# Kernel tuning notes

Measured on AMD Instinct MI355X. Metric: run time of the kernel, lower is better.

Reference implementation:

```python
import jax, jax.numpy as jnp
import numpy as np

F_REP = 256
F_BET = 512
N_PER = 6
MAGNITUDE = 0.001


def _glorot(key, shape):
    fan_in = shape[0]
    return jax.random.normal(key, shape, dtype=jnp.float32) / np.sqrt(fan_in)


def setup_inputs() -> dict:
    key = jax.random.key(0)
    ks = jax.random.split(key, 24)
    n_atoms, n_tors = 50000, 300000
    inp = {
        'h': jax.random.normal(ks[0], (n_atoms, F_REP), dtype=jnp.float32),
        'idxs': jax.random.randint(ks[1], (n_tors, 4), 0, n_atoms, dtype=jnp.int64),
        # symmetrizer: skippedLinear(4*rep, bet) + DenseBlock(bet, depth=3)
        'Ws0': _glorot(ks[2], (4 * F_REP, F_BET)), 'bs0': jnp.zeros((F_BET,), jnp.float32),
        'Ws1': _glorot(ks[3], (F_BET, F_BET)), 'bs1': jnp.zeros((F_BET,), jnp.float32),
        'Ws2': _glorot(ks[4], (F_BET, F_BET)), 'bs2': jnp.zeros((F_BET,), jnp.float32),
        'Ws3': _glorot(ks[5], (F_BET, F_BET)), 'bs3': jnp.zeros((F_BET,), jnp.float32),
        # torsion_nn: DenseBlock(bet, depth=2) + Linear(bet, n_periodicity)
        'Wt0': _glorot(ks[6], (F_BET, F_BET)), 'bt0': jnp.zeros((F_BET,), jnp.float32),
        'Wt1': _glorot(ks[7], (F_BET, F_BET)), 'bt1': jnp.zeros((F_BET,), jnp.float32),
        'Wt2': _glorot(ks[8], (F_BET, N_PER)), 'bt2': jnp.zeros((N_PER,), jnp.float32),
        # classification_nn: skippedLinear(bet, bet) + Linear(bet, n_periodicity)
        'Wc0': _glorot(ks[9], (F_BET, F_BET)), 'bc0': jnp.zeros((F_BET,), jnp.float32),
        'Wc1': _glorot(ks[10], (F_BET, N_PER)), 'bc1': jnp.zeros((N_PER,), jnp.float32),
    }
    return inp


def _symmetrizer(x, Ws0, bs0, Ws1, bs1, Ws2, bs2, Ws3, bs3):
    # skippedLinear(4*rep, bet): dims differ -> plain Linear + ELU
    h = jax.nn.elu(x @ Ws0 + bs0)
    # DenseBlock: residual Linear+ELU layers (in==out)
    for W, b in ((Ws1, bs1), (Ws2, bs2), (Ws3, bs3)):
        h = h + jax.nn.elu(h @ W + b)
    return h


def reference(h, idxs, Ws0, bs0, Ws1, bs1, Ws2, bs2, Ws3, bs3,
              Wt0, bt0, Wt1, bt1, Wt2, bt2, Wc0, bc0, Wc1, bc1):
    feats = h[idxs]  # [N, 4, F_REP] gather
    f1, f2, f3, f4 = feats[:, 0], feats[:, 1], feats[:, 2], feats[:, 3]
    x_fwd = jnp.concatenate([f1, f2, f3, f4], axis=-1)  # [N, 4F]
    x_rev = jnp.concatenate([f4, f3, f2, f1], axis=-1)
    sym = (_symmetrizer(x_fwd, Ws0, bs0, Ws1, bs1, Ws2, bs2, Ws3, bs3)
           + _symmetrizer(x_rev, Ws0, bs0, Ws1, bs1, Ws2, bs2, Ws3, bs3))
    # torsion_nn
    t = sym + jax.nn.elu(sym @ Wt0 + bt0)
    t = t + jax.nn.elu(t @ Wt1 + bt1)
    coeffs = t @ Wt2 + bt2  # [N, n_periodicity]
    # classification_nn (skippedLinear with in==out -> residual)
    c = sym + jax.nn.elu(sym @ Wc0 + bc0)
    score = c @ Wc1 + bc1  # [N, n_periodicity]
    gate = jax.nn.sigmoid(score)  # hardness == 1
    k = coeffs * MAGNITUDE * gate
    return jnp.stack([score, k])  # [2, N, n_periodicity]
```

## Files before the change

kernel.cpp:

```cpp
#include <hip/hip_runtime.h>

#define BM 64
#define NTHREADS 512
#define BM4 32
#define NT4 1024

typedef __attribute__((ext_vector_type(8))) short short8;
typedef __attribute__((ext_vector_type(4))) float f32x4;

__device__ __forceinline__ short f2bf(float f) {
  unsigned u = __builtin_bit_cast(unsigned, f);
  u += 0x7FFFu + ((u >> 16) & 1u);
  return (short)(u >> 16);
}
__device__ __forceinline__ float bf2f(short s) {
  unsigned u = ((unsigned)(unsigned short)s) << 16;
  return __builtin_bit_cast(float, u);
}
__device__ __forceinline__ float elu_f(float v) {
  return v > 0.f ? v : (__expf(v) - 1.f);
}

__global__ __launch_bounds__(256) void pack_w(const float* __restrict__ src,
                                              short* __restrict__ dst,
                                              int K, int N, int rev) {
  int tile = blockIdx.x * 4 + (threadIdx.x >> 6);
  int lane = threadIdx.x & 63;
  int ktiles = K >> 5;
  int tot = (N >> 4) * ktiles;
  if (tile >= tot) return;
  int nt = tile / ktiles, kt = tile - nt * ktiles;
  int col = (nt << 4) + (lane & 15);
  int k0 = (kt << 5) + ((lane >> 4) << 3);
  short8 o;
#pragma unroll
  for (int j = 0; j < 8; ++j) {
    int kr = k0 + j;
    if (rev) kr = ((3 - (kr >> 8)) << 8) | (kr & 255);
    o[j] = f2bf(src[(size_t)kr * N + col]);
  }
  *(short8*)(dst + (size_t)tile * 512 + lane * 8) = o;
}

__device__ __forceinline__ short8 ldg_bfrag(const short* W, int ktiles, int ct,
                                            int kt, int lane) {
  return *(const short8*)(W + ((size_t)(ct * ktiles + kt) << 9) + (lane << 3));
}

__device__ __forceinline__ int swz(int row, int boff) {
  return row * 1024 + (boff ^ ((row & 7) << 4) ^ (((row >> 3) & 1) << 7));
}
__device__ __forceinline__ short8 lds_a32(const char* base, int rt, int kt, int lane) {
  int row = rt * 16 + (lane & 15);
  int boff = (kt << 6) + ((lane >> 4) << 4);
  return *(const short8*)(base + swz(row, boff));
}

__device__ __forceinline__ short8 lds_afrag64(const char* base, int stride, int rt,
                                              int kt, int lane) {
  int row = rt * 16 + (lane & 15);
  int boff = (kt << 6) + ((lane >> 4) << 4);
  return *(const short8*)(base + row * stride + (boff ^ ((row & 7) << 4)));
}

__global__ __launch_bounds__(NTHREADS) void atom_pre(const float* __restrict__ h,
                                                     const short* __restrict__ W0f,
                                                     short* __restrict__ p,
                                                     int n_atoms) {
  __shared__ char sh[BM * 512];
  const int tid = threadIdx.x, lane = tid & 63, wv = tid >> 6;
  const int r0 = blockIdx.x * BM;
  for (int i = tid; i < BM * 32; i += NTHREADS) {
    int row = i >> 5, c0 = (i & 31) << 3;
    int ga = r0 + row;
    short8 o;
    if (ga < n_atoms) {
      const float4* s4 = (const float4*)(h + (size_t)ga * 256 + c0);
      float4 v0 = s4[0], v1 = s4[1];
      o[0] = f2bf(v0.x); o[1] = f2bf(v0.y); o[2] = f2bf(v0.z); o[3] = f2bf(v0.w);
      o[4] = f2bf(v1.x); o[5] = f2bf(v1.y); o[6] = f2bf(v1.z); o[7] = f2bf(v1.w);
    } else {
#pragma unroll
      for (int e = 0; e < 8; ++e) o[e] = 0;
    }
    *(short8*)(sh + row * 512 + ((c0 * 2) ^ ((row & 7) << 4))) = o;
  }
  __syncthreads();
#pragma unroll 1
  for (int s = 0; s < 4; ++s) {
    f32x4 acc[4][4];
    const f32x4 z = {0.f, 0.f, 0.f, 0.f};
#pragma unroll
    for (int rt = 0; rt < 4; ++rt)
#pragma unroll
      for (int cf = 0; cf < 4; ++cf) acc[rt][cf] = z;
    for (int kt = 0; kt < 8; ++kt) {
      short8 a[4], b[4];
#pragma unroll
      for (int rt = 0; rt < 4; ++rt) a[rt] = lds_afrag64(sh, 512, rt, kt, lane);
#pragma unroll
      for (int cf = 0; cf < 4; ++cf)
        b[cf] = ldg_bfrag(W0f, 32, (wv << 2) + cf, (s << 3) + kt, lane);
#pragma unroll
      for (int rt = 0; rt < 4; ++rt)
#pragma unroll
        for (int cf = 0; cf < 4; ++cf)
          acc[rt][cf] = __builtin_amdgcn_mfma_f32_16x16x32_bf16(a[rt], b[cf], acc[rt][cf], 0, 0, 0);
    }
#pragma unroll
    for (int rt = 0; rt < 4; ++rt)
#pragma unroll
      for (int cf = 0; cf < 4; ++cf) {
        int col = (wv << 6) + (cf << 4) + (lane & 15);
#pragma unroll
        for (int i = 0; i < 4; ++i) {
          int row = rt * 16 + ((lane >> 4) << 2) + i;
          int ga = r0 + row;
          if (ga < n_atoms) p[((size_t)ga * 4 + s) * 512 + col] = f2bf(acc[rt][cf][i]);
        }
      }
  }
}

struct P2 {
  const int* idxs;
  const short* p;
  const short *W1, *W2, *W3, *Wt0, *Wt1, *Wc0;
  const float *bs0, *bs1, *bs2, *bs3, *bt0, *bt1, *bt2, *bc0, *bc1;
  const float *Wt2, *Wc1;
  float* out;
  int n_tors;
};


__device__ __forceinline__ void mfma_dual(const char* sA, const char* sB,
                                          const short* __restrict__ W,
                                          const float* __restrict__ bias,
                                          f32x4 (&accf)[2][2], f32x4 (&accr)[2][2],
                                          int wv, int lane) {
  float b0 = bias[(wv << 5) + (lane & 15)];
  float b1 = bias[(wv << 5) + 16 + (lane & 15)];
#pragma unroll
  for (int rt = 0; rt < 2; ++rt) {
    accf[rt][0] = (f32x4){b0, b0, b0, b0};
    accf[rt][1] = (f32x4){b1, b1, b1, b1};
    accr[rt][0] = (f32x4){b0, b0, b0, b0};
    accr[rt][1] = (f32x4){b1, b1, b1, b1};
  }
  short8 bC[2], bN[2];
#pragma unroll
  for (int cf = 0; cf < 2; ++cf) bC[cf] = ldg_bfrag(W, 16, (wv << 1) + cf, 0, lane);
#pragma unroll 1
  for (int kt = 0; kt < 16; ++kt) {
#pragma unroll
    for (int cf = 0; cf < 2; ++cf)
      bN[cf] = ldg_bfrag(W, 16, (wv << 1) + cf, (kt + 1) & 15, lane);
#pragma unroll
    for (int rt = 0; rt < 2; ++rt) {
      short8 af = lds_a32(sA, rt, kt, lane);
      short8 ar = lds_a32(sB, rt, kt, lane);
#pragma unroll
      for (int cf = 0; cf < 2; ++cf) {
        accf[rt][cf] = __builtin_amdgcn_mfma_f32_16x16x32_bf16(af, bC[cf], accf[rt][cf], 0, 0, 0);
        accr[rt][cf] = __builtin_amdgcn_mfma_f32_16x16x32_bf16(ar, bC[cf], accr[rt][cf], 0, 0, 0);
      }
    }
#pragma unroll
    for (int cf = 0; cf < 2; ++cf) bC[cf] = bN[cf];
  }
}

__device__ __forceinline__ void mfma_dualB(const char* sA,
                                           const short* __restrict__ Wa,
                                           const short* __restrict__ Wb,
                                           const float* __restrict__ ba,
                                           const float* __restrict__ bb,
                                           f32x4 (&accA)[2][2], f32x4 (&accB)[2][2],
                                           int wv, int lane) {
  float a0 = ba[(wv << 5) + (lane & 15)];
  float a1 = ba[(wv << 5) + 16 + (lane & 15)];
  float c0 = bb[(wv << 5) + (lane & 15)];
  float c1 = bb[(wv << 5) + 16 + (lane & 15)];
#pragma unroll
  for (int rt = 0; rt < 2; ++rt) {
    accA[rt][0] = (f32x4){a0, a0, a0, a0};
    accA[rt][1] = (f32x4){a1, a1, a1, a1};
    accB[rt][0] = (f32x4){c0, c0, c0, c0};
    accB[rt][1] = (f32x4){c1, c1, c1, c1};
  }
#pragma unroll 1
  for (int kt = 0; kt < 16; ++kt) {
    short8 bA[2], bB[2];
#pragma unroll
    for (int cf = 0; cf < 2; ++cf) {
      bA[cf] = ldg_bfrag(Wa, 16, (wv << 1) + cf, kt, lane);
      bB[cf] = ldg_bfrag(Wb, 16, (wv << 1) + cf, kt, lane);
    }
#pragma unroll
    for (int rt = 0; rt < 2; ++rt) {
      short8 a = lds_a32(sA, rt, kt, lane);
#pragma unroll
      for (int cf = 0; cf < 2; ++cf) {
        accA[rt][cf] = __builtin_amdgcn_mfma_f32_16x16x32_bf16(a, bA[cf], accA[rt][cf], 0, 0, 0);
        accB[rt][cf] = __builtin_amdgcn_mfma_f32_16x16x32_bf16(a, bB[cf], accB[rt][cf], 0, 0, 0);
      }
    }
  }
}

__device__ __forceinline__ void mfma_single(const char* src,
                                            const short* __restrict__ W,
                                            const float* __restrict__ bias,
                                            f32x4 (&acc)[2][2], int wv, int lane) {
  float b0 = bias[(wv << 5) + (lane & 15)];
  float b1 = bias[(wv << 5) + 16 + (lane & 15)];
#pragma unroll
  for (int rt = 0; rt < 2; ++rt) {
    acc[rt][0] = (f32x4){b0, b0, b0, b0};
    acc[rt][1] = (f32x4){b1, b1, b1, b1};
  }
  short8 bC[2], bN[2];
#pragma unroll
  for (int cf = 0; cf < 2; ++cf) bC[cf] = ldg_bfrag(W, 16, (wv << 1) + cf, 0, lane);
#pragma unroll 1
  for (int kt = 0; kt < 16; ++kt) {
#pragma unroll
    for (int cf = 0; cf < 2; ++cf)
      bN[cf] = ldg_bfrag(W, 16, (wv << 1) + cf, (kt + 1) & 15, lane);
#pragma unroll
    for (int rt = 0; rt < 2; ++rt) {
      short8 a = lds_a32(src, rt, kt, lane);
#pragma unroll
      for (int cf = 0; cf < 2; ++cf)
        acc[rt][cf] = __builtin_amdgcn_mfma_f32_16x16x32_bf16(a, bC[cf], acc[rt][cf], 0, 0, 0);
    }
#pragma unroll
    for (int cf = 0; cf < 2; ++cf) bC[cf] = bN[cf];
  }
}

__global__ __launch_bounds__(NT4, 8) void fused4(P2 p) {
  __shared__ char sA[BM4 * 1024];
  __shared__ char sB[BM4 * 1024];
  __shared__ int sIdx[BM4 * 4];
  __shared__ float sSmall[BM4 * 12];
  const int tid = threadIdx.x;
  const int lane = tid & 63;
  const int wv = tid >> 6;
  const int r0 = blockIdx.x * BM4;

  if (tid < BM4 * 4) {
    int grow = r0 + (tid >> 2);
    sIdx[tid] = (grow < p.n_tors) ? p.idxs[(size_t)grow * 4 + (tid & 3)] : 0;
  }
  __syncthreads();

#pragma unroll 1
  for (int i = tid; i < BM4 * 64; i += NT4) {
    int row = i >> 6, c0 = (i & 63) << 3;
    float sf[8], sr[8];
#pragma unroll
    for (int e = 0; e < 8; ++e) { sf[e] = p.bs0[c0 + e]; sr[e] = sf[e]; }
#pragma unroll
    for (int j = 0; j < 4; ++j) {
      int a = sIdx[row * 4 + j];
      short8 vf = *(const short8*)(p.p + ((size_t)a * 4 + j) * 512 + c0);
      short8 vr = *(const short8*)(p.p + ((size_t)a * 4 + (3 - j)) * 512 + c0);
#pragma unroll
      for (int e = 0; e < 8; ++e) { sf[e] += bf2f(vf[e]); sr[e] += bf2f(vr[e]); }
    }
    short8 of, orv;
#pragma unroll
    for (int e = 0; e < 8; ++e) { of[e] = f2bf(elu_f(sf[e])); orv[e] = f2bf(elu_f(sr[e])); }
    int off = swz(row, c0 * 2);
    *(short8*)(sA + off) = of;
    *(short8*)(sB + off) = orv;
  }
  __syncthreads();

  f32x4 accA[2][2], accB[2][2];

  const short* Ws[3] = {p.W1, p.W2, p.W3};
  const float* bs[3] = {p.bs1, p.bs2, p.bs3};
#pragma unroll 1
  for (int L = 0; L < 3; ++L) {
    mfma_dual(sA, sB, Ws[L], bs[L], accA, accB, wv, lane);
    __syncthreads();
#pragma unroll
    for (int rt = 0; rt < 2; ++rt)
#pragma unroll
      for (int cf = 0; cf < 2; ++cf) {
        int col = (wv << 5) + (cf << 4) + (lane & 15);
#pragma unroll
        for (int i = 0; i < 4; ++i) {
          int row = rt * 16 + ((lane >> 4) << 2) + i;
          int off = swz(row, col * 2);
          short* pf = (short*)(sA + off);
          short* pr = (short*)(sB + off);
          float nf = bf2f(*pf) + elu_f(accA[rt][cf][i]);
          float nr = bf2f(*pr) + elu_f(accB[rt][cf][i]);
          if (L == 2) {
            *pf = f2bf(nf + nr);
          } else {
            *pf = f2bf(nf);
            *pr = f2bf(nr);
          }
        }
      }
    __syncthreads();
  }

  mfma_dualB(sA, p.Wt0, p.Wc0, p.bt0, p.bc0, accA, accB, wv, lane);
  __syncthreads();
#pragma unroll
  for (int rt = 0; rt < 2; ++rt)
#pragma unroll
    for (int cf = 0; cf < 2; ++cf) {
      int col = (wv << 5) + (cf << 4) + (lane & 15);
#pragma unroll
      for (int i = 0; i < 4; ++i) {
        int row = rt * 16 + ((lane >> 4) << 2) + i;
        int off = swz(row, col * 2);
        float s = bf2f(*(short*)(sA + off));
        *(short*)(sB + off) = f2bf(s + elu_f(accA[rt][cf][i]));
        *(short*)(sA + off) = f2bf(s + elu_f(accB[rt][cf][i]));
      }
    }
  __syncthreads();

  mfma_single(sB, p.Wt1, p.bt1, accA, wv, lane);
  __syncthreads();
#pragma unroll
  for (int rt = 0; rt < 2; ++rt)
#pragma unroll
    for (int cf = 0; cf < 2; ++cf) {
      int col = (wv << 5) + (cf << 4) + (lane & 15);
#pragma unroll
      for (int i = 0; i < 4; ++i) {
        int row = rt * 16 + ((lane >> 4) << 2) + i;
        int off = swz(row, col * 2);
        short* pt = (short*)(sB + off);
        *pt = f2bf(bf2f(*pt) + elu_f(accA[rt][cf][i]));
      }
    }
  __syncthreads();

  if (tid < BM4 * 12) {
    int row = tid / 12, jj = tid - row * 12;
    int j = (jj < 6) ? jj : jj - 6;
    const char* src = (jj < 6) ? sB : sA;
    const float* W = (jj < 6) ? p.Wt2 : p.Wc1;
    float acc = (jj < 6) ? p.bt2[j] : p.bc1[j];
#pragma unroll 1
    for (int c0 = 0; c0 < 512; c0 += 8) {
      short8 v = *(const short8*)(src + swz(row, c0 * 2));
#pragma unroll
      for (int e = 0; e < 8; ++e) acc += bf2f(v[e]) * W[(c0 + e) * 6 + j];
    }
    sSmall[row * 12 + jj] = acc;
  }
  __syncthreads();
  if (tid < BM4 * 6) {
    int row = tid / 6, j = tid - row * 6;
    int grow = r0 + row;
    if (grow < p.n_tors) {
      float score = sSmall[row * 12 + 6 + j];
      float coeff = sSmall[row * 12 + j];
      p.out[(size_t)grow * 6 + j] = score;
      p.out[(size_t)p.n_tors * 6 + (size_t)grow * 6 + j] =
          coeff * 0.001f * (1.0f / (1.0f + __expf(-score)));
    }
  }
}


struct Params {
  const float* h;
  const int* idxs;
  const short *W0f, *W0r, *W1, *W2, *W3, *Wt0, *Wt1, *Wc0;
  const float *bs0, *bs1, *bs2, *bs3, *bt0, *bt1, *bt2, *bc0, *bc1;
  const float *Wt2, *Wc1;
  float* out;
  int n_tors;
};

__device__ __forceinline__ void layer_dual(char* hf, char* hr,
                                           const short* __restrict__ W,
                                           const float* __restrict__ bias,
                                           int wv, int lane) {
  f32x4 accf[4][4], accr[4][4];
  const f32x4 z = {0.f, 0.f, 0.f, 0.f};
#pragma unroll
  for (int rt = 0; rt < 4; ++rt)
#pragma unroll
    for (int cf = 0; cf < 4; ++cf) { accf[rt][cf] = z; accr[rt][cf] = z; }
  for (int kt = 0; kt < 16; ++kt) {
    short8 af[4], ar[4], b[4];
#pragma unroll
    for (int rt = 0; rt < 4; ++rt) {
      af[rt] = lds_afrag64(hf, 1024, rt, kt, lane);
      ar[rt] = lds_afrag64(hr, 1024, rt, kt, lane);
    }
#pragma unroll
    for (int cf = 0; cf < 4; ++cf) b[cf] = ldg_bfrag(W, 16, (wv << 2) + cf, kt, lane);
#pragma unroll
    for (int rt = 0; rt < 4; ++rt)
#pragma unroll
      for (int cf = 0; cf < 4; ++cf) {
        accf[rt][cf] = __builtin_amdgcn_mfma_f32_16x16x32_bf16(af[rt], b[cf], accf[rt][cf], 0, 0, 0);
        accr[rt][cf] = __builtin_amdgcn_mfma_f32_16x16x32_bf16(ar[rt], b[cf], accr[rt][cf], 0, 0, 0);
      }
  }
  float bcol[4];
#pragma unroll
  for (int cf = 0; cf < 4; ++cf) bcol[cf] = bias[(wv << 6) + (cf << 4) + (lane & 15)];
  __syncthreads();
#pragma unroll
  for (int rt = 0; rt < 4; ++rt)
#pragma unroll
    for (int cf = 0; cf < 4; ++cf) {
      int col = (wv << 6) + (cf << 4) + (lane & 15);
#pragma unroll
      for (int i = 0; i < 4; ++i) {
        int row = rt * 16 + ((lane >> 4) << 2) + i;
        size_t off = (size_t)row * 1024 + ((col * 2) ^ ((row & 7) << 4));
        short* pf = (short*)(hf + off);
        short* pr = (short*)(hr + off);
        *pf = f2bf(bf2f(*pf) + elu_f(accf[rt][cf][i] + bcol[cf]));
        *pr = f2bf(bf2f(*pr) + elu_f(accr[rt][cf][i] + bcol[cf]));
      }
    }
  __syncthreads();
}

__device__ __forceinline__ void layer_single(const char* in,
                                             const short* __restrict__ W,
                                             const float* __restrict__ bias,
                                             const char* res, char* out,
                                             int wv, int lane) {
  f32x4 acc[4][4];
  const f32x4 z = {0.f, 0.f, 0.f, 0.f};
#pragma unroll
  for (int rt = 0; rt < 4; ++rt)
#pragma unroll
    for (int cf = 0; cf < 4; ++cf) acc[rt][cf] = z;
  for (int kt = 0; kt < 16; ++kt) {
    short8 a[4], b[4];
#pragma unroll
    for (int rt = 0; rt < 4; ++rt) a[rt] = lds_afrag64(in, 1024, rt, kt, lane);
#pragma unroll
    for (int cf = 0; cf < 4; ++cf) b[cf] = ldg_bfrag(W, 16, (wv << 2) + cf, kt, lane);
#pragma unroll
    for (int rt = 0; rt < 4; ++rt)
#pragma unroll
      for (int cf = 0; cf < 4; ++cf)
        acc[rt][cf] = __builtin_amdgcn_mfma_f32_16x16x32_bf16(a[rt], b[cf], acc[rt][cf], 0, 0, 0);
  }
  float bcol[4];
#pragma unroll
  for (int cf = 0; cf < 4; ++cf) bcol[cf] = bias[(wv << 6) + (cf << 4) + (lane & 15)];
  __syncthreads();
#pragma unroll
  for (int rt = 0; rt < 4; ++rt)
#pragma unroll
    for (int cf = 0; cf < 4; ++cf) {
      int col = (wv << 6) + (cf << 4) + (lane & 15);
#pragma unroll
      for (int i = 0; i < 4; ++i) {
        int row = rt * 16 + ((lane >> 4) << 2) + i;
        size_t off = (size_t)row * 1024 + ((col * 2) ^ ((row & 7) << 4));
        float v = elu_f(acc[rt][cf][i] + bcol[cf]) + bf2f(*(const short*)(res + off));
        *(short*)(out + off) = f2bf(v);
      }
    }
  __syncthreads();
}

__global__ __launch_bounds__(NTHREADS) void fused(Params p) {
  __shared__ char smem[BM * 2048];
  __shared__ float sSmall[BM * 12];
  char* sA = smem;
  char* sB = smem + BM * 1024;
  const int tid = threadIdx.x;
  const int lane = tid & 63;
  const int wv = tid >> 6;
  const int r0 = blockIdx.x * BM;

  for (int c = tid; c < BM * 128; c += NTHREADS) {
    int row = c >> 7;
    int col0 = (c & 127) << 3;
    int grow = r0 + row;
    short8 o;
    if (grow < p.n_tors) {
      int f = col0 >> 8;
      int cin = col0 & 255;
      int a = p.idxs[(size_t)grow * 4 + f];
      const float4* s4 = (const float4*)(p.h + (size_t)a * 256 + cin);
      float4 v0 = s4[0], v1 = s4[1];
      o[0] = f2bf(v0.x); o[1] = f2bf(v0.y); o[2] = f2bf(v0.z); o[3] = f2bf(v0.w);
      o[4] = f2bf(v1.x); o[5] = f2bf(v1.y); o[6] = f2bf(v1.z); o[7] = f2bf(v1.w);
    } else {
#pragma unroll
      for (int e = 0; e < 8; ++e) o[e] = 0;
    }
    *(short8*)(smem + (size_t)row * 2048 + ((col0 * 2) ^ ((row & 7) << 4))) = o;
  }
  __syncthreads();

  {
    f32x4 accf[4][4], accr[4][4];
    const f32x4 z = {0.f, 0.f, 0.f, 0.f};
#pragma unroll
    for (int rt = 0; rt < 4; ++rt)
#pragma unroll
      for (int cf = 0; cf < 4; ++cf) { accf[rt][cf] = z; accr[rt][cf] = z; }
    for (int kt = 0; kt < 32; ++kt) {
      short8 a[4], bfw[4], brw[4];
#pragma unroll
      for (int rt = 0; rt < 4; ++rt) a[rt] = lds_afrag64(smem, 2048, rt, kt, lane);
#pragma unroll
      for (int cf = 0; cf < 4; ++cf) {
        bfw[cf] = ldg_bfrag(p.W0f, 32, (wv << 2) + cf, kt, lane);
        brw[cf] = ldg_bfrag(p.W0r, 32, (wv << 2) + cf, kt, lane);
      }
#pragma unroll
      for (int rt = 0; rt < 4; ++rt)
#pragma unroll
        for (int cf = 0; cf < 4; ++cf) {
          accf[rt][cf] = __builtin_amdgcn_mfma_f32_16x16x32_bf16(a[rt], bfw[cf], accf[rt][cf], 0, 0, 0);
          accr[rt][cf] = __builtin_amdgcn_mfma_f32_16x16x32_bf16(a[rt], brw[cf], accr[rt][cf], 0, 0, 0);
        }
    }
    float bcol[4];
#pragma unroll
    for (int cf = 0; cf < 4; ++cf) bcol[cf] = p.bs0[(wv << 6) + (cf << 4) + (lane & 15)];
    __syncthreads();
#pragma unroll
    for (int rt = 0; rt < 4; ++rt)
#pragma unroll
      for (int cf = 0; cf < 4; ++cf) {
        int col = (wv << 6) + (cf << 4) + (lane & 15);
#pragma unroll
        for (int i = 0; i < 4; ++i) {
          int row = rt * 16 + ((lane >> 4) << 2) + i;
          size_t off = (size_t)row * 1024 + ((col * 2) ^ ((row & 7) << 4));
          *(short*)(sA + off) = f2bf(elu_f(accf[rt][cf][i] + bcol[cf]));
          *(short*)(sB + off) = f2bf(elu_f(accr[rt][cf][i] + bcol[cf]));
        }
      }
    __syncthreads();
  }

  layer_dual(sA, sB, p.W1, p.bs1, wv, lane);
  layer_dual(sA, sB, p.W2, p.bs2, wv, lane);
  layer_dual(sA, sB, p.W3, p.bs3, wv, lane);

  for (int c = tid; c < BM * 64; c += NTHREADS) {
    int row = c >> 6;
    int col0 = (c & 63) << 3;
    size_t off = (size_t)row * 1024 + ((col0 * 2) ^ ((row & 7) << 4));
    short8 xa = *(short8*)(sA + off);
    short8 xb = *(short8*)(sB + off);
    short8 o;
#pragma unroll
    for (int e = 0; e < 8; ++e) o[e] = f2bf(bf2f(xa[e]) + bf2f(xb[e]));
    *(short8*)(sA + off) = o;
  }
  __syncthreads();

  layer_single(sA, p.Wt0, p.bt0, sA, sB, wv, lane);
  layer_single(sB, p.Wt1, p.bt1, sB, sB, wv, lane);
  layer_single(sA, p.Wc0, p.bc0, sA, sA, wv, lane);

  for (int idx = tid; idx < BM * 12; idx += NTHREADS) {
    int row = idx / 12, jj = idx - row * 12;
    int j = (jj < 6) ? jj : jj - 6;
    const char* src = (jj < 6) ? sB : sA;
    const float* W = (jj < 6) ? p.Wt2 : p.Wc1;
    float acc = (jj < 6) ? p.bt2[j] : p.bc1[j];
    for (int c0 = 0; c0 < 512; c0 += 8) {
      short8 v = *(const short8*)(src + (size_t)row * 1024 + ((c0 * 2) ^ ((row & 7) << 4)));
#pragma unroll
      for (int e = 0; e < 8; ++e) acc += bf2f(v[e]) * W[(c0 + e) * 6 + j];
    }
    sSmall[row * 12 + jj] = acc;
  }
  __syncthreads();
  for (int idx = tid; idx < BM * 6; idx += NTHREADS) {
    int row = idx / 6, j = idx - row * 6;
    int grow = r0 + row;
    if (grow < p.n_tors) {
      float score = sSmall[row * 12 + 6 + j];
      float coeff = sSmall[row * 12 + j];
      p.out[(size_t)grow * 6 + j] = score;
      p.out[(size_t)p.n_tors * 6 + (size_t)grow * 6 + j] =
          coeff * 0.001f * (1.0f / (1.0f + __expf(-score)));
    }
  }
}


extern "C" void kernel_launch(void* const* d_in, const int* in_sizes, int n_in,
                              void* d_out, int out_size, void* d_ws, size_t ws_size,
                              hipStream_t stream) {
  const float* h   = (const float*)d_in[0];
  const int* idxs  = (const int*)d_in[1];
  const float* Ws0 = (const float*)d_in[2];
  const float* bs0 = (const float*)d_in[3];
  const float* Ws1 = (const float*)d_in[4];
  const float* bs1 = (const float*)d_in[5];
  const float* Ws2 = (const float*)d_in[6];
  const float* bs2 = (const float*)d_in[7];
  const float* Ws3 = (const float*)d_in[8];
  const float* bs3 = (const float*)d_in[9];
  const float* Wt0 = (const float*)d_in[10];
  const float* bt0 = (const float*)d_in[11];
  const float* Wt1 = (const float*)d_in[12];
  const float* bt1 = (const float*)d_in[13];
  const float* Wt2 = (const float*)d_in[14];
  const float* bt2 = (const float*)d_in[15];
  const float* Wc0 = (const float*)d_in[16];
  const float* bc0 = (const float*)d_in[17];
  const float* Wc1 = (const float*)d_in[18];
  const float* bc1 = (const float*)d_in[19];
  int n_tors = in_sizes[1] / 4;
  int n_atoms = in_sizes[0] / 256;

  auto pk = [&](const float* s, short* dmem, int K, int N, int rev) {
    int tiles = (N >> 4) * (K >> 5);
    pack_w<<<dim3((tiles + 3) / 4), dim3(256), 0, stream>>>(s, dmem, K, N, rev);
  };

  size_t pElems = (size_t)n_atoms * 4 * 512;
  size_t needNew = (pElems + 524288 + 6 * 262144) * sizeof(short);

  if (ws_size >= needNew) {
    short* ws = (short*)d_ws;
    short* pT  = ws;
    short* W0f = ws + pElems;
    short* W1  = W0f + 524288;
    short* W2  = W1 + 262144;
    short* W3  = W2 + 262144;
    short* Wt0c = W3 + 262144;
    short* Wt1c = Wt0c + 262144;
    short* Wc0c = Wt1c + 262144;

    pk(Ws0, W0f, 1024, 512, 0);
    pk(Ws1, W1, 512, 512, 0);
    pk(Ws2, W2, 512, 512, 0);
    pk(Ws3, W3, 512, 512, 0);
    pk(Wt0, Wt0c, 512, 512, 0);
    pk(Wt1, Wt1c, 512, 512, 0);
    pk(Wc0, Wc0c, 512, 512, 0);

    atom_pre<<<dim3((n_atoms + BM - 1) / BM), dim3(NTHREADS), 0, stream>>>(h, W0f, pT, n_atoms);

    P2 p;
    p.idxs = idxs; p.p = pT;
    p.W1 = W1; p.W2 = W2; p.W3 = W3;
    p.Wt0 = Wt0c; p.Wt1 = Wt1c; p.Wc0 = Wc0c;
    p.bs0 = bs0; p.bs1 = bs1; p.bs2 = bs2; p.bs3 = bs3;
    p.bt0 = bt0; p.bt1 = bt1; p.bt2 = bt2; p.bc0 = bc0; p.bc1 = bc1;
    p.Wt2 = Wt2; p.Wc1 = Wc1;
    p.out = (float*)d_out; p.n_tors = n_tors;

    fused4<<<dim3((n_tors + BM4 - 1) / BM4), dim3(NT4), 0, stream>>>(p);
  } else {
    short* ws = (short*)d_ws;
    short* W0f = ws;
    short* W0r = ws + 524288;
    short* W1  = ws + 1048576;
    short* W2  = W1 + 262144;
    short* W3  = W2 + 262144;
    short* Wt0c = W3 + 262144;
    short* Wt1c = Wt0c + 262144;
    short* Wc0c = Wt1c + 262144;

    pk(Ws0, W0f, 1024, 512, 0);
    pk(Ws0, W0r, 1024, 512, 1);
    pk(Ws1, W1, 512, 512, 0);
    pk(Ws2, W2, 512, 512, 0);
    pk(Ws3, W3, 512, 512, 0);
    pk(Wt0, Wt0c, 512, 512, 0);
    pk(Wt1, Wt1c, 512, 512, 0);
    pk(Wc0, Wc0c, 512, 512, 0);

    Params p;
    p.h = h; p.idxs = idxs;
    p.W0f = W0f; p.W0r = W0r; p.W1 = W1; p.W2 = W2; p.W3 = W3;
    p.Wt0 = Wt0c; p.Wt1 = Wt1c; p.Wc0 = Wc0c;
    p.bs0 = bs0; p.bs1 = bs1; p.bs2 = bs2; p.bs3 = bs3;
    p.bt0 = bt0; p.bt1 = bt1; p.bt2 = bt2; p.bc0 = bc0; p.bc1 = bc1;
    p.Wt2 = Wt2; p.Wc1 = Wc1;
    p.out = (float*)d_out; p.n_tors = n_tors;

    fused<<<dim3((n_tors + BM - 1) / BM), dim3(NTHREADS), 0, stream>>>(p);
  }
}
```

Baseline: 3.065 ms.

## Switch fused torsion MLP to 32x32x16 MFMA with fragment-ordered LDS layout

Replaces the 16x16x32 bf16 MFMA tiles in the fused per-torsion MLP with 32x32x16 MFMA tiles. Each wave now covers the full 32-row block and 64 columns, so the block shrinks from 1024 to 512 threads. Weights are repacked into 32-column fragments, and the LDS activation buffers are stored in MFMA A-fragment order so each k-step reads them with one contiguous vector load. The goal is fewer LDS A-fragment reads and less weight traffic per FLOP. In exchange, accumulator register pressure rises and there are fewer waves per block to hide latency.

```diff
diff --git a/kernel.cpp b/kernel.cpp
--- a/kernel.cpp
+++ b/kernel.cpp
@@ -3,10 +3,11 @@
 #define BM 64
 #define NTHREADS 512
 #define BM4 32
-#define NT4 1024
+#define NT5 512
 
 typedef __attribute__((ext_vector_type(8))) short short8;
 typedef __attribute__((ext_vector_type(4))) float f32x4;
+typedef __attribute__((ext_vector_type(16))) float f32x16;
 
 __device__ __forceinline__ short f2bf(float f) {
   unsigned u = __builtin_bit_cast(unsigned, f);
@@ -42,18 +43,26 @@
   *(short8*)(dst + (size_t)tile * 512 + lane * 8) = o;
 }
 
+__global__ __launch_bounds__(256) void pack_w32(const float* __restrict__ src,
+                                                short* __restrict__ dst,
+                                                int K, int N) {
+  int tile = blockIdx.x * 4 + (threadIdx.x >> 6);
+  int lane = threadIdx.x & 63;
+  int ktiles = K >> 4;
+  int tot = (N >> 5) * ktiles;
+  if (tile >= tot) return;
+  int nt = tile / ktiles, kt = tile - nt * ktiles;
+  int col = (nt << 5) + (lane & 31);
+  int k0 = (kt << 4) + ((lane >> 5) << 3);
+  short8 o;
+#pragma unroll
+  for (int j = 0; j < 8; ++j) o[j] = f2bf(src[(size_t)(k0 + j) * N + col]);
+  *(short8*)(dst + (size_t)tile * 512 + lane * 8) = o;
+}
+
 __device__ __forceinline__ short8 ldg_bfrag(const short* W, int ktiles, int ct,
                                             int kt, int lane) {
   return *(const short8*)(W + ((size_t)(ct * ktiles + kt) << 9) + (lane << 3));
-}
-
-__device__ __forceinline__ int swz(int row, int boff) {
-  return row * 1024 + (boff ^ ((row & 7) << 4) ^ (((row >> 3) & 1) << 7));
-}
-__device__ __forceinline__ short8 lds_a32(const char* base, int rt, int kt, int lane) {
-  int row = rt * 16 + (lane & 15);
-  int boff = (kt << 6) + ((lane >> 4) << 4);
-  return *(const short8*)(base + swz(row, boff));
 }
 
 __device__ __forceinline__ short8 lds_afrag64(const char* base, int stride, int rt,
@@ -132,114 +141,102 @@
   int n_tors;
 };
 
-
-__device__ __forceinline__ void mfma_dual(const char* sA, const char* sB,
-                                          const short* __restrict__ W,
-                                          const float* __restrict__ bias,
-                                          f32x4 (&accf)[2][2], f32x4 (&accr)[2][2],
-                                          int wv, int lane) {
-  float b0 = bias[(wv << 5) + (lane & 15)];
-  float b1 = bias[(wv << 5) + 16 + (lane & 15)];
-#pragma unroll
-  for (int rt = 0; rt < 2; ++rt) {
-    accf[rt][0] = (f32x4){b0, b0, b0, b0};
-    accf[rt][1] = (f32x4){b1, b1, b1, b1};
-    accr[rt][0] = (f32x4){b0, b0, b0, b0};
-    accr[rt][1] = (f32x4){b1, b1, b1, b1};
-  }
-  short8 bC[2], bN[2];
-#pragma unroll
-  for (int cf = 0; cf < 2; ++cf) bC[cf] = ldg_bfrag(W, 16, (wv << 1) + cf, 0, lane);
-#pragma unroll 1
-  for (int kt = 0; kt < 16; ++kt) {
-#pragma unroll
-    for (int cf = 0; cf < 2; ++cf)
-      bN[cf] = ldg_bfrag(W, 16, (wv << 1) + cf, (kt + 1) & 15, lane);
-#pragma unroll
-    for (int rt = 0; rt < 2; ++rt) {
-      short8 af = lds_a32(sA, rt, kt, lane);
-      short8 ar = lds_a32(sB, rt, kt, lane);
-#pragma unroll
-      for (int cf = 0; cf < 2; ++cf) {
-        accf[rt][cf] = __builtin_amdgcn_mfma_f32_16x16x32_bf16(af, bC[cf], accf[rt][cf], 0, 0, 0);
-        accr[rt][cf] = __builtin_amdgcn_mfma_f32_16x16x32_bf16(ar, bC[cf], accr[rt][cf], 0, 0, 0);
-      }
-    }
-#pragma unroll
-    for (int cf = 0; cf < 2; ++cf) bC[cf] = bN[cf];
-  }
-}
-
-__device__ __forceinline__ void mfma_dualB(const char* sA,
-                                           const short* __restrict__ Wa,
-                                           const short* __restrict__ Wb,
-                                           const float* __restrict__ ba,
-                                           const float* __restrict__ bb,
-                                           f32x4 (&accA)[2][2], f32x4 (&accB)[2][2],
-                                           int wv, int lane) {
-  float a0 = ba[(wv << 5) + (lane & 15)];
-  float a1 = ba[(wv << 5) + 16 + (lane & 15)];
-  float c0 = bb[(wv << 5) + (lane & 15)];
-  float c1 = bb[(wv << 5) + 16 + (lane & 15)];
-#pragma unroll
-  for (int rt = 0; rt < 2; ++rt) {
-    accA[rt][0] = (f32x4){a0, a0, a0, a0};
-    accA[rt][1] = (f32x4){a1, a1, a1, a1};
-    accB[rt][0] = (f32x4){c0, c0, c0, c0};
-    accB[rt][1] = (f32x4){c1, c1, c1, c1};
-  }
-#pragma unroll 1
-  for (int kt = 0; kt < 16; ++kt) {
-    short8 bA[2], bB[2];
-#pragma unroll
-    for (int cf = 0; cf < 2; ++cf) {
-      bA[cf] = ldg_bfrag(Wa, 16, (wv << 1) + cf, kt, lane);
-      bB[cf] = ldg_bfrag(Wb, 16, (wv << 1) + cf, kt, lane);
-    }
-#pragma unroll
-    for (int rt = 0; rt < 2; ++rt) {
-      short8 a = lds_a32(sA, rt, kt, lane);
-#pragma unroll
-      for (int cf = 0; cf < 2; ++cf) {
-        accA[rt][cf] = __builtin_amdgcn_mfma_f32_16x16x32_bf16(a, bA[cf], accA[rt][cf], 0, 0, 0);
-        accB[rt][cf] = __builtin_amdgcn_mfma_f32_16x16x32_bf16(a, bB[cf], accB[rt][cf], 0, 0, 0);
-      }
-    }
-  }
-}
-
-__device__ __forceinline__ void mfma_single(const char* src,
+__device__ __forceinline__ int fragoff(int r, int c) {
+  return ((c >> 4) << 10) + (((r & 31) + (((c >> 3) & 1) << 5)) << 4) + ((c & 7) << 1);
+}
+__device__ __forceinline__ short8 lds_a(const char* base, int kt, int lane) {
+  return *(const short8*)(base + (kt << 10) + (lane << 4));
+}
+
+__device__ __forceinline__ void mfma_dual32(const char* sA, const char* sB,
                                             const short* __restrict__ W,
                                             const float* __restrict__ bias,
-                                            f32x4 (&acc)[2][2], int wv, int lane) {
-  float b0 = bias[(wv << 5) + (lane & 15)];
-  float b1 = bias[(wv << 5) + 16 + (lane & 15)];
-#pragma unroll
-  for (int rt = 0; rt < 2; ++rt) {
-    acc[rt][0] = (f32x4){b0, b0, b0, b0};
-    acc[rt][1] = (f32x4){b1, b1, b1, b1};
+                                            f32x16 (&aF)[2], f32x16 (&aR)[2],
+                                            int wv, int lane) {
+  float b0 = bias[(wv << 6) + (lane & 31)];
+  float b1 = bias[(wv << 6) + 32 + (lane & 31)];
+#pragma unroll
+  for (int i = 0; i < 16; ++i) {
+    aF[0][i] = b0; aF[1][i] = b1; aR[0][i] = b0; aR[1][i] = b1;
   }
   short8 bC[2], bN[2];
 #pragma unroll
-  for (int cf = 0; cf < 2; ++cf) bC[cf] = ldg_bfrag(W, 16, (wv << 1) + cf, 0, lane);
+  for (int cf = 0; cf < 2; ++cf) bC[cf] = ldg_bfrag(W, 32, (wv << 1) + cf, 0, lane);
 #pragma unroll 1
-  for (int kt = 0; kt < 16; ++kt) {
+  for (int kt = 0; kt < 32; ++kt) {
 #pragma unroll
     for (int cf = 0; cf < 2; ++cf)
-      bN[cf] = ldg_bfrag(W, 16, (wv << 1) + cf, (kt + 1) & 15, lane);
-#pragma unroll
-    for (int rt = 0; rt < 2; ++rt) {
-      short8 a = lds_a32(src, rt, kt, lane);
-#pragma unroll
-      for (int cf = 0; cf < 2; ++cf)
-        acc[rt][cf] = __builtin_amdgcn_mfma_f32_16x16x32_bf16(a, bC[cf], acc[rt][cf], 0, 0, 0);
+      bN[cf] = ldg_bfrag(W, 32, (wv << 1) + cf, (kt + 1) & 31, lane);
+    short8 af = lds_a(sA, kt, lane);
+    short8 ar = lds_a(sB, kt, lane);
+#pragma unroll
+    for (int cf = 0; cf < 2; ++cf) {
+      aF[cf] = __builtin_amdgcn_mfma_f32_32x32x16_bf16(af, bC[cf], aF[cf], 0, 0, 0);
+      aR[cf] = __builtin_amdgcn_mfma_f32_32x32x16_bf16(ar, bC[cf], aR[cf], 0, 0, 0);
     }
 #pragma unroll
     for (int cf = 0; cf < 2; ++cf) bC[cf] = bN[cf];
   }
 }
 
-__global__ __launch_bounds__(NT4, 8) void fused4(P2 p) {
+__device__ __forceinline__ void mfma_dualB32(const char* sA,
+                                             const short* __restrict__ Wa,
+                                             const short* __restrict__ Wb,
+                                             const float* __restrict__ ba,
+                                             const float* __restrict__ bb,
+                                             f32x16 (&aA)[2], f32x16 (&aB)[2],
+                                             int wv, int lane) {
+  float a0 = ba[(wv << 6) + (lane & 31)];
+  float a1 = ba[(wv << 6) + 32 + (lane & 31)];
+  float c0 = bb[(wv << 6) + (lane & 31)];
+  float c1 = bb[(wv << 6) + 32 + (lane & 31)];
+#pragma unroll
+  for (int i = 0; i < 16; ++i) {
+    aA[0][i] = a0; aA[1][i] = a1; aB[0][i] = c0; aB[1][i] = c1;
+  }
+#pragma unroll 1
+  for (int kt = 0; kt < 32; ++kt) {
+    short8 bA[2], bB[2];
+#pragma unroll
+    for (int cf = 0; cf < 2; ++cf) {
+      bA[cf] = ldg_bfrag(Wa, 32, (wv << 1) + cf, kt, lane);
+      bB[cf] = ldg_bfrag(Wb, 32, (wv << 1) + cf, kt, lane);
+    }
+    short8 a = lds_a(sA, kt, lane);
+#pragma unroll
+    for (int cf = 0; cf < 2; ++cf) {
+      aA[cf] = __builtin_amdgcn_mfma_f32_32x32x16_bf16(a, bA[cf], aA[cf], 0, 0, 0);
+      aB[cf] = __builtin_amdgcn_mfma_f32_32x32x16_bf16(a, bB[cf], aB[cf], 0, 0, 0);
+    }
+  }
+}
+
+__device__ __forceinline__ void mfma_single32(const char* src,
+                                              const short* __restrict__ W,
+                                              const float* __restrict__ bias,
+                                              f32x16 (&acc)[2], int wv, int lane) {
+  float b0 = bias[(wv << 6) + (lane & 31)];
+  float b1 = bias[(wv << 6) + 32 + (lane & 31)];
+#pragma unroll
+  for (int i = 0; i < 16; ++i) { acc[0][i] = b0; acc[1][i] = b1; }
+  short8 bC[2], bN[2];
+#pragma unroll
+  for (int cf = 0; cf < 2; ++cf) bC[cf] = ldg_bfrag(W, 32, (wv << 1) + cf, 0, lane);
+#pragma unroll 1
+  for (int kt = 0; kt < 32; ++kt) {
+#pragma unroll
+    for (int cf = 0; cf < 2; ++cf)
+      bN[cf] = ldg_bfrag(W, 32, (wv << 1) + cf, (kt + 1) & 31, lane);
+    short8 a = lds_a(src, kt, lane);
+#pragma unroll
+    for (int cf = 0; cf < 2; ++cf)
+      acc[cf] = __builtin_amdgcn_mfma_f32_32x32x16_bf16(a, bC[cf], acc[cf], 0, 0, 0);
+#pragma unroll
+    for (int cf = 0; cf < 2; ++cf) bC[cf] = bN[cf];
+  }
+}
+
+__global__ __launch_bounds__(NT5, 4) void fused5(P2 p) {
   __shared__ char sA[BM4 * 1024];
   __shared__ char sB[BM4 * 1024];
   __shared__ int sIdx[BM4 * 4];
@@ -256,7 +253,7 @@
   __syncthreads();
 
 #pragma unroll 1
-  for (int i = tid; i < BM4 * 64; i += NT4) {
+  for (int i = tid; i < BM4 * 64; i += NT5) {
     int row = i >> 6, c0 = (i & 63) << 3;
     float sf[8], sr[8];
 #pragma unroll
@@ -272,77 +269,71 @@
     short8 of, orv;
 #pragma unroll
     for (int e = 0; e < 8; ++e) { of[e] = f2bf(elu_f(sf[e])); orv[e] = f2bf(elu_f(sr[e])); }
-    int off = swz(row, c0 * 2);
+    int off = fragoff(row, c0);
     *(short8*)(sA + off) = of;
     *(short8*)(sB + off) = orv;
   }
   __syncthreads();
 
-  f32x4 accA[2][2], accB[2][2];
+  f32x16 accF[2], accR[2];
 
   const short* Ws[3] = {p.W1, p.W2, p.W3};
   const float* bs[3] = {p.bs1, p.bs2, p.bs3};
 #pragma unroll 1
   for (int L = 0; L < 3; ++L) {
-    mfma_dual(sA, sB, Ws[L], bs[L], accA, accB, wv, lane);
+    mfma_dual32(sA, sB, Ws[L], bs[L], accF, accR, wv, lane);
     __syncthreads();
 #pragma unroll
-    for (int rt = 0; rt < 2; ++rt)
-#pragma unroll
-      for (int cf = 0; cf < 2; ++cf) {
-        int col = (wv << 5) + (cf << 4) + (lane & 15);
-#pragma unroll
-        for (int i = 0; i < 4; ++i) {
-          int row = rt * 16 + ((lane >> 4) << 2) + i;
-          int off = swz(row, col * 2);
-          short* pf = (short*)(sA + off);
-          short* pr = (short*)(sB + off);
-          float nf = bf2f(*pf) + elu_f(accA[rt][cf][i]);
-          float nr = bf2f(*pr) + elu_f(accB[rt][cf][i]);
-          if (L == 2) {
-            *pf = f2bf(nf + nr);
-          } else {
-            *pf = f2bf(nf);
-            *pr = f2bf(nr);
-          }
+    for (int cf = 0; cf < 2; ++cf) {
+      int c = (wv << 6) + (cf << 5) + (lane & 31);
+#pragma unroll
+      for (int i = 0; i < 16; ++i) {
+        int r = (i & 3) + ((i >> 2) << 3) + ((lane >> 5) << 2);
+        int off = fragoff(r, c);
+        short* pf = (short*)(sA + off);
+        short* pr = (short*)(sB + off);
+        float nf = bf2f(*pf) + elu_f(accF[cf][i]);
+        float nr = bf2f(*pr) + elu_f(accR[cf][i]);
+        if (L == 2) {
+          *pf = f2bf(nf + nr);
+        } else {
+          *pf = f2bf(nf);
+          *pr = f2bf(nr);
         }
       }
+    }
     __syncthreads();
   }
 
-  mfma_dualB(sA, p.Wt0, p.Wc0, p.bt0, p.bc0, accA, accB, wv, lane);
-  __syncthreads();
-#pragma unroll
-  for (int rt = 0; rt < 2; ++rt)
-#pragma unroll
-    for (int cf = 0; cf < 2; ++cf) {
-      int col = (wv << 5) + (cf << 4) + (lane & 15);
-#pragma unroll
-      for (int i = 0; i < 4; ++i) {
-        int row = rt * 16 + ((lane >> 4) << 2) + i;
-        int off = swz(row, col * 2);
-        float s = bf2f(*(short*)(sA + off));
-        *(short*)(sB + off) = f2bf(s + elu_f(accA[rt][cf][i]));
-        *(short*)(sA + off) = f2bf(s + elu_f(accB[rt][cf][i]));
-      }
-    }
-  __syncthreads();
-
-  mfma_single(sB, p.Wt1, p.bt1, accA, wv, lane);
-  __syncthreads();
-#pragma unroll
-  for (int rt = 0; rt < 2; ++rt)
-#pragma unroll
-    for (int cf = 0; cf < 2; ++cf) {
-      int col = (wv << 5) + (cf << 4) + (lane & 15);
-#pragma unroll
-      for (int i = 0; i < 4; ++i) {
-        int row = rt * 16 + ((lane >> 4) << 2) + i;
-        int off = swz(row, col * 2);
-        short* pt = (short*)(sB + off);
-        *pt = f2bf(bf2f(*pt) + elu_f(accA[rt][cf][i]));
-      }
-    }
+  mfma_dualB32(sA, p.Wt0, p.Wc0, p.bt0, p.bc0, accF, accR, wv, lane);
+  __syncthreads();
+#pragma unroll
+  for (int cf = 0; cf < 2; ++cf) {
+    int c = (wv << 6) + (cf << 5) + (lane & 31);
+#pragma unroll
+    for (int i = 0; i < 16; ++i) {
+      int r = (i & 3) + ((i >> 2) << 3) + ((lane >> 5) << 2);
+      int off = fragoff(r, c);
+      float s = bf2f(*(short*)(sA + off));
+      *(short*)(sB + off) = f2bf(s + elu_f(accF[cf][i]));
+      *(short*)(sA + off) = f2bf(s + elu_f(accR[cf][i]));
+    }
+  }
+  __syncthreads();
+
+  mfma_single32(sB, p.Wt1, p.bt1, accF, wv, lane);
+  __syncthreads();
+#pragma unroll
+  for (int cf = 0; cf < 2; ++cf) {
+    int c = (wv << 6) + (cf << 5) + (lane & 31);
+#pragma unroll
+    for (int i = 0; i < 16; ++i) {
+      int r = (i & 3) + ((i >> 2) << 3) + ((lane >> 5) << 2);
+      int off = fragoff(r, c);
+      short* pt = (short*)(sB + off);
+      *pt = f2bf(bf2f(*pt) + elu_f(accF[cf][i]));
+    }
+  }
   __syncthreads();
 
   if (tid < BM4 * 12) {
@@ -353,7 +344,7 @@
     float acc = (jj < 6) ? p.bt2[j] : p.bc1[j];
 #pragma unroll 1
     for (int c0 = 0; c0 < 512; c0 += 8) {
-      short8 v = *(const short8*)(src + swz(row, c0 * 2));
+      short8 v = *(const short8*)(src + fragoff(row, c0));
 #pragma unroll
       for (int e = 0; e < 8; ++e) acc += bf2f(v[e]) * W[(c0 + e) * 6 + j];
     }
@@ -630,6 +621,10 @@
     int tiles = (N >> 4) * (K >> 5);
     pack_w<<<dim3((tiles + 3) / 4), dim3(256), 0, stream>>>(s, dmem, K, N, rev);
   };
+  auto pk32 = [&](const float* s, short* dmem, int K, int N) {
+    int tiles = (N >> 5) * (K >> 4);
+    pack_w32<<<dim3((tiles + 3) / 4), dim3(256), 0, stream>>>(s, dmem, K, N);
+  };
 
   size_t pElems = (size_t)n_atoms * 4 * 512;
   size_t needNew = (pElems + 524288 + 6 * 262144) * sizeof(short);
@@ -646,12 +641,12 @@
     short* Wc0c = Wt1c + 262144;
 
     pk(Ws0, W0f, 1024, 512, 0);
-    pk(Ws1, W1, 512, 512, 0);
-    pk(Ws2, W2, 512, 512, 0);
-    pk(Ws3, W3, 512, 512, 0);
-    pk(Wt0, Wt0c, 512, 512, 0);
-    pk(Wt1, Wt1c, 512, 512, 0);
-    pk(Wc0, Wc0c, 512, 512, 0);
+    pk32(Ws1, W1, 512, 512);
+    pk32(Ws2, W2, 512, 512);
+    pk32(Ws3, W3, 512, 512);
+    pk32(Wt0, Wt0c, 512, 512);
+    pk32(Wt1, Wt1c, 512, 512);
+    pk32(Wc0, Wc0c, 512, 512);
 
     atom_pre<<<dim3((n_atoms + BM - 1) / BM), dim3(NTHREADS), 0, stream>>>(h, W0f, pT, n_atoms);
 
@@ -664,7 +659,7 @@
     p.Wt2 = Wt2; p.Wc1 = Wc1;
     p.out = (float*)d_out; p.n_tors = n_tors;
 
-    fused4<<<dim3((n_tors + BM4 - 1) / BM4), dim3(NT4), 0, stream>>>(p);
+    fused5<<<dim3((n_tors + BM4 - 1) / BM4), dim3(NT5), 0, stream>>>(p);
   } else {
     short* ws = (short*)d_ws;
     short* W0f = ws;
```

Result: slower. 3.490 ms (+13.9%).

## Halve block threads so each wave computes 64 output columns

Applied to the files above, without the earlier changes.

The fused torsion kernel drops from 1024 to 512 threads per block, so each of the 8 waves now computes a 32x64 output tile (4 column fragments) instead of 32x32. Each LDS A-fragment load is reused across twice as many MFMAs, which cuts LDS traffic and per-wave overhead. In exchange, accumulator register use per wave doubles and the launch bound falls from 8 to 4 blocks per CU, which may reduce latency hiding.

```diff
diff --git a/kernel.cpp b/kernel.cpp
--- a/kernel.cpp
+++ b/kernel.cpp
@@ -3,7 +3,7 @@
 #define BM 64
 #define NTHREADS 512
 #define BM4 32
-#define NT4 1024
+#define NT7 512
 
 typedef __attribute__((ext_vector_type(8))) short short8;
 typedef __attribute__((ext_vector_type(4))) float f32x4;
@@ -133,113 +133,117 @@
 };
 
 
-__device__ __forceinline__ void mfma_dual(const char* sA, const char* sB,
-                                          const short* __restrict__ W,
-                                          const float* __restrict__ bias,
-                                          f32x4 (&accf)[2][2], f32x4 (&accr)[2][2],
-                                          int wv, int lane) {
-  float b0 = bias[(wv << 5) + (lane & 15)];
-  float b1 = bias[(wv << 5) + 16 + (lane & 15)];
-#pragma unroll
-  for (int rt = 0; rt < 2; ++rt) {
-    accf[rt][0] = (f32x4){b0, b0, b0, b0};
-    accf[rt][1] = (f32x4){b1, b1, b1, b1};
-    accr[rt][0] = (f32x4){b0, b0, b0, b0};
-    accr[rt][1] = (f32x4){b1, b1, b1, b1};
-  }
-  short8 bC[2], bN[2];
-#pragma unroll
-  for (int cf = 0; cf < 2; ++cf) bC[cf] = ldg_bfrag(W, 16, (wv << 1) + cf, 0, lane);
+__device__ __forceinline__ void mfma_dual7(const char* sA, const char* sB,
+                                           const short* __restrict__ W,
+                                           const float* __restrict__ bias,
+                                           f32x4 (&aF)[2][4], f32x4 (&aR)[2][4],
+                                           int wv, int lane) {
+  float b[4];
+#pragma unroll
+  for (int cf = 0; cf < 4; ++cf) b[cf] = bias[(wv << 6) + (cf << 4) + (lane & 15)];
+#pragma unroll
+  for (int rt = 0; rt < 2; ++rt)
+#pragma unroll
+    for (int cf = 0; cf < 4; ++cf) {
+      aF[rt][cf] = (f32x4){b[cf], b[cf], b[cf], b[cf]};
+      aR[rt][cf] = (f32x4){b[cf], b[cf], b[cf], b[cf]};
+    }
+  short8 bC[4], bN[4];
+#pragma unroll
+  for (int cf = 0; cf < 4; ++cf) bC[cf] = ldg_bfrag(W, 16, (wv << 2) + cf, 0, lane);
 #pragma unroll 1
   for (int kt = 0; kt < 16; ++kt) {
 #pragma unroll
-    for (int cf = 0; cf < 2; ++cf)
-      bN[cf] = ldg_bfrag(W, 16, (wv << 1) + cf, (kt + 1) & 15, lane);
+    for (int cf = 0; cf < 4; ++cf)
+      bN[cf] = ldg_bfrag(W, 16, (wv << 2) + cf, (kt + 1) & 15, lane);
+    short8 af[2], ar[2];
 #pragma unroll
     for (int rt = 0; rt < 2; ++rt) {
-      short8 af = lds_a32(sA, rt, kt, lane);
-      short8 ar = lds_a32(sB, rt, kt, lane);
-#pragma unroll
-      for (int cf = 0; cf < 2; ++cf) {
-        accf[rt][cf] = __builtin_amdgcn_mfma_f32_16x16x32_bf16(af, bC[cf], accf[rt][cf], 0, 0, 0);
-        accr[rt][cf] = __builtin_amdgcn_mfma_f32_16x16x32_bf16(ar, bC[cf], accr[rt][cf], 0, 0, 0);
-      }
-    }
-#pragma unroll
-    for (int cf = 0; cf < 2; ++cf) bC[cf] = bN[cf];
-  }
-}
-
-__device__ __forceinline__ void mfma_dualB(const char* sA,
-                                           const short* __restrict__ Wa,
-                                           const short* __restrict__ Wb,
-                                           const float* __restrict__ ba,
-                                           const float* __restrict__ bb,
-                                           f32x4 (&accA)[2][2], f32x4 (&accB)[2][2],
-                                           int wv, int lane) {
-  float a0 = ba[(wv << 5) + (lane & 15)];
-  float a1 = ba[(wv << 5) + 16 + (lane & 15)];
-  float c0 = bb[(wv << 5) + (lane & 15)];
-  float c1 = bb[(wv << 5) + 16 + (lane & 15)];
-#pragma unroll
-  for (int rt = 0; rt < 2; ++rt) {
-    accA[rt][0] = (f32x4){a0, a0, a0, a0};
-    accA[rt][1] = (f32x4){a1, a1, a1, a1};
-    accB[rt][0] = (f32x4){c0, c0, c0, c0};
-    accB[rt][1] = (f32x4){c1, c1, c1, c1};
+      af[rt] = lds_a32(sA, rt, kt, lane);
+      ar[rt] = lds_a32(sB, rt, kt, lane);
+    }
+#pragma unroll
+    for (int rt = 0; rt < 2; ++rt)
+#pragma unroll
+      for (int cf = 0; cf < 4; ++cf) {
+        aF[rt][cf] = __builtin_amdgcn_mfma_f32_16x16x32_bf16(af[rt], bC[cf], aF[rt][cf], 0, 0, 0);
+        aR[rt][cf] = __builtin_amdgcn_mfma_f32_16x16x32_bf16(ar[rt], bC[cf], aR[rt][cf], 0, 0, 0);
+      }
+#pragma unroll
+    for (int cf = 0; cf < 4; ++cf) bC[cf] = bN[cf];
+  }
+}
+
+__device__ __forceinline__ void mfma_dualB7(const char* sA,
+                                            const short* __restrict__ Wa,
+                                            const short* __restrict__ Wb,
+                                            const float* __restrict__ ba,
+                                            const float* __restrict__ bb,
+                                            f32x4 (&aA)[2][4], f32x4 (&aB)[2][4],
+                                            int wv, int lane) {
+#pragma unroll
+  for (int cf = 0; cf < 4; ++cf) {
+    float va = ba[(wv << 6) + (cf << 4) + (lane & 15)];
+    float vb = bb[(wv << 6) + (cf << 4) + (lane & 15)];
+#pragma unroll
+    for (int rt = 0; rt < 2; ++rt) {
+      aA[rt][cf] = (f32x4){va, va, va, va};
+      aB[rt][cf] = (f32x4){vb, vb, vb, vb};
+    }
   }
 #pragma unroll 1
   for (int kt = 0; kt < 16; ++kt) {
-    short8 bA[2], bB[2];
-#pragma unroll
-    for (int cf = 0; cf < 2; ++cf) {
-      bA[cf] = ldg_bfrag(Wa, 16, (wv << 1) + cf, kt, lane);
-      bB[cf] = ldg_bfrag(Wb, 16, (wv << 1) + cf, kt, lane);
-    }
-#pragma unroll
-    for (int rt = 0; rt < 2; ++rt) {
-      short8 a = lds_a32(sA, rt, kt, lane);
-#pragma unroll
-      for (int cf = 0; cf < 2; ++cf) {
-        accA[rt][cf] = __builtin_amdgcn_mfma_f32_16x16x32_bf16(a, bA[cf], accA[rt][cf], 0, 0, 0);
-        accB[rt][cf] = __builtin_amdgcn_mfma_f32_16x16x32_bf16(a, bB[cf], accB[rt][cf], 0, 0, 0);
-      }
-    }
-  }
-}
-
-__device__ __forceinline__ void mfma_single(const char* src,
-                                            const short* __restrict__ W,
-                                            const float* __restrict__ bias,
-                                            f32x4 (&acc)[2][2], int wv, int lane) {
-  float b0 = bias[(wv << 5) + (lane & 15)];
-  float b1 = bias[(wv << 5) + 16 + (lane & 15)];
-#pragma unroll
-  for (int rt = 0; rt < 2; ++rt) {
-    acc[rt][0] = (f32x4){b0, b0, b0, b0};
-    acc[rt][1] = (f32x4){b1, b1, b1, b1};
-  }
-  short8 bC[2], bN[2];
-#pragma unroll
-  for (int cf = 0; cf < 2; ++cf) bC[cf] = ldg_bfrag(W, 16, (wv << 1) + cf, 0, lane);
+    short8 bA[4], bB[4];
+#pragma unroll
+    for (int cf = 0; cf < 4; ++cf) {
+      bA[cf] = ldg_bfrag(Wa, 16, (wv << 2) + cf, kt, lane);
+      bB[cf] = ldg_bfrag(Wb, 16, (wv << 2) + cf, kt, lane);
+    }
+    short8 a[2];
+#pragma unroll
+    for (int rt = 0; rt < 2; ++rt) a[rt] = lds_a32(sA, rt, kt, lane);
+#pragma unroll
+    for (int rt = 0; rt < 2; ++rt)
+#pragma unroll
+      for (int cf = 0; cf < 4; ++cf) {
+        aA[rt][cf] = __builtin_amdgcn_mfma_f32_16x16x32_bf16(a[rt], bA[cf], aA[rt][cf], 0, 0, 0);
+        aB[rt][cf] = __builtin_amdgcn_mfma_f32_16x16x32_bf16(a[rt], bB[cf], aB[rt][cf], 0, 0, 0);
+      }
+  }
+}
+
+__device__ __forceinline__ void mfma_single7(const char* src,
+                                             const short* __restrict__ W,
+                                             const float* __restrict__ bias,
+                                             f32x4 (&acc)[2][4], int wv, int lane) {
+#pragma unroll
+  for (int cf = 0; cf < 4; ++cf) {
+    float b = bias[(wv << 6) + (cf << 4) + (lane & 15)];
+#pragma unroll
+    for (int rt = 0; rt < 2; ++rt) acc[rt][cf] = (f32x4){b, b, b, b};
+  }
+  short8 bC[4], bN[4];
+#pragma unroll
+  for (int cf = 0; cf < 4; ++cf) bC[cf] = ldg_bfrag(W, 16, (wv << 2) + cf, 0, lane);
 #pragma unroll 1
   for (int kt = 0; kt < 16; ++kt) {
 #pragma unroll
-    for (int cf = 0; cf < 2; ++cf)
-      bN[cf] = ldg_bfrag(W, 16, (wv << 1) + cf, (kt + 1) & 15, lane);
-#pragma unroll
-    for (int rt = 0; rt < 2; ++rt) {
-      short8 a = lds_a32(src, rt, kt, lane);
-#pragma unroll
-      for (int cf = 0; cf < 2; ++cf)
-        acc[rt][cf] = __builtin_amdgcn_mfma_f32_16x16x32_bf16(a, bC[cf], acc[rt][cf], 0, 0, 0);
-    }
-#pragma unroll
-    for (int cf = 0; cf < 2; ++cf) bC[cf] = bN[cf];
-  }
-}
-
-__global__ __launch_bounds__(NT4, 8) void fused4(P2 p) {
+    for (int cf = 0; cf < 4; ++cf)
+      bN[cf] = ldg_bfrag(W, 16, (wv << 2) + cf, (kt + 1) & 15, lane);
+    short8 a[2];
+#pragma unroll
+    for (int rt = 0; rt < 2; ++rt) a[rt] = lds_a32(src, rt, kt, lane);
+#pragma unroll
+    for (int rt = 0; rt < 2; ++rt)
+#pragma unroll
+      for (int cf = 0; cf < 4; ++cf)
+        acc[rt][cf] = __builtin_amdgcn_mfma_f32_16x16x32_bf16(a[rt], bC[cf], acc[rt][cf], 0, 0, 0);
+#pragma unroll
+    for (int cf = 0; cf < 4; ++cf) bC[cf] = bN[cf];
+  }
+}
+
+__global__ __launch_bounds__(NT7, 4) void fused7(P2 p) {
   __shared__ char sA[BM4 * 1024];
   __shared__ char sB[BM4 * 1024];
   __shared__ int sIdx[BM4 * 4];
@@ -256,7 +260,7 @@
   __syncthreads();
 
 #pragma unroll 1
-  for (int i = tid; i < BM4 * 64; i += NT4) {
+  for (int i = tid; i < BM4 * 64; i += NT7) {
     int row = i >> 6, c0 = (i & 63) << 3;
     float sf[8], sr[8];
 #pragma unroll
@@ -278,27 +282,27 @@
   }
   __syncthreads();
 
-  f32x4 accA[2][2], accB[2][2];
+  f32x4 accF[2][4], accR[2][4];
 
   const short* Ws[3] = {p.W1, p.W2, p.W3};
   const float* bs[3] = {p.bs1, p.bs2, p.bs3};
 #pragma unroll 1
   for (int L = 0; L < 3; ++L) {
-    mfma_dual(sA, sB, Ws[L], bs[L], accA, accB, wv, lane);
+    mfma_dual7(sA, sB, Ws[L], bs[L], accF, accR, wv, lane);
     __syncthreads();
 #pragma unroll
     for (int rt = 0; rt < 2; ++rt)
 #pragma unroll
-      for (int cf = 0; cf < 2; ++cf) {
-        int col = (wv << 5) + (cf << 4) + (lane & 15);
+      for (int cf = 0; cf < 4; ++cf) {
+        int col = (wv << 6) + (cf << 4) + (lane & 15);
 #pragma unroll
         for (int i = 0; i < 4; ++i) {
           int row = rt * 16 + ((lane >> 4) << 2) + i;
           int off = swz(row, col * 2);
           short* pf = (short*)(sA + off);
           short* pr = (short*)(sB + off);
-          float nf = bf2f(*pf) + elu_f(accA[rt][cf][i]);
-          float nr = bf2f(*pr) + elu_f(accB[rt][cf][i]);
+          float nf = bf2f(*pf) + elu_f(accF[rt][cf][i]);
+          float nr = bf2f(*pr) + elu_f(accR[rt][cf][i]);
           if (L == 2) {
             *pf = f2bf(nf + nr);
           } else {
@@ -310,37 +314,37 @@
     __syncthreads();
   }
 
-  mfma_dualB(sA, p.Wt0, p.Wc0, p.bt0, p.bc0, accA, accB, wv, lane);
+  mfma_dualB7(sA, p.Wt0, p.Wc0, p.bt0, p.bc0, accF, accR, wv, lane);
   __syncthreads();
 #pragma unroll
   for (int rt = 0; rt < 2; ++rt)
 #pragma unroll
-    for (int cf = 0; cf < 2; ++cf) {
-      int col = (wv << 5) + (cf << 4) + (lane & 15);
+    for (int cf = 0; cf < 4; ++cf) {
+      int col = (wv << 6) + (cf << 4) + (lane & 15);
 #pragma unroll
       for (int i = 0; i < 4; ++i) {
         int row = rt * 16 + ((lane >> 4) << 2) + i;
         int off = swz(row, col * 2);
         float s = bf2f(*(short*)(sA + off));
-        *(short*)(sB + off) = f2bf(s + elu_f(accA[rt][cf][i]));
-        *(short*)(sA + off) = f2bf(s + elu_f(accB[rt][cf][i]));
-      }
-    }
-  __syncthreads();
-
-  mfma_single(sB, p.Wt1, p.bt1, accA, wv, lane);
+        *(short*)(sB + off) = f2bf(s + elu_f(accF[rt][cf][i]));
+        *(short*)(sA + off) = f2bf(s + elu_f(accR[rt][cf][i]));
+      }
+    }
+  __syncthreads();
+
+  mfma_single7(sB, p.Wt1, p.bt1, accF, wv, lane);
   __syncthreads();
 #pragma unroll
   for (int rt = 0; rt < 2; ++rt)
 #pragma unroll
-    for (int cf = 0; cf < 2; ++cf) {
-      int col = (wv << 5) + (cf << 4) + (lane & 15);
+    for (int cf = 0; cf < 4; ++cf) {
+      int col = (wv << 6) + (cf << 4) + (lane & 15);
 #pragma unroll
       for (int i = 0; i < 4; ++i) {
         int row = rt * 16 + ((lane >> 4) << 2) + i;
         int off = swz(row, col * 2);
         short* pt = (short*)(sB + off);
-        *pt = f2bf(bf2f(*pt) + elu_f(accA[rt][cf][i]));
+        *pt = f2bf(bf2f(*pt) + elu_f(accF[rt][cf][i]));
       }
     }
   __syncthreads();
@@ -664,7 +668,7 @@
     p.Wt2 = Wt2; p.Wc1 = Wc1;
     p.out = (float*)d_out; p.n_tors = n_tors;
 
-    fused4<<<dim3((n_tors + BM4 - 1) / BM4), dim3(NT4), 0, stream>>>(p);
+    fused7<<<dim3((n_tors + BM4 - 1) / BM4), dim3(NT7), 0, stream>>>(p);
   } else {
     short* ws = (short*)d_ws;
     short* W0f = ws;
```

Result: faster. 3.004 ms (-2.0%).
